# Kernel optimization log

Measured on AMD Instinct MI355X. Metric: run time of the kernel, lower is better.

Reference implementation:

```python
import jax, jax.numpy as jnp
import numpy as np

H = 1024        # bridge_hidden_dim
NH = 16         # num_attention_heads
HD = H // NH    # head_dim = 64
B, S = 4, 1024
PHYS_W = 0.2
CONS_W = 0.15


def setup_inputs() -> dict:
    key = jax.random.key(0)
    ks = jax.random.split(key, 16)
    sc = 0.02
    return {
        "cnn_features": jax.random.normal(ks[0], (B, S, H), jnp.float32),
        "llm_features": jax.random.normal(ks[1], (B, S, H), jnp.float32),
        "Wq": jax.random.normal(ks[2], (H, H), jnp.float32) * sc,
        "bq": jnp.zeros((H,), jnp.float32),
        "Wk": jax.random.normal(ks[3], (H, H), jnp.float32) * sc,
        "bk": jnp.zeros((H,), jnp.float32),
        "Wv": jax.random.normal(ks[4], (H, H), jnp.float32) * sc,
        "bv": jnp.zeros((H,), jnp.float32),
        "Wo": jax.random.normal(ks[5], (H, H), jnp.float32) * sc,
        "bo": jnp.zeros((H,), jnp.float32),
        "ln_g": jnp.ones((H,), jnp.float32),
        "ln_b": jnp.zeros((H,), jnp.float32),
        "e_energy": jax.random.normal(ks[6], (H,), jnp.float32),
        "e_mass": jax.random.normal(ks[7], (H,), jnp.float32),
        "e_momentum": jax.random.normal(ks[8], (H,), jnp.float32),
    }


def _layernorm(x, g, b, eps=1e-5):
    mu = jnp.mean(x, axis=-1, keepdims=True)
    var = jnp.var(x, axis=-1, keepdims=True)
    return (x - mu) * jax.lax.rsqrt(var + eps) * g + b


def _split_heads(x):
    b, s, _ = x.shape
    return x.reshape(b, s, NH, HD).transpose(0, 2, 1, 3)  # [b, h, s, d]


def _physics_attention(q_in, k_in, v_in, Wq, bq, Wk, bk, Wv, bv, Wo, bo, ln_g, ln_b):
    # q_in: [b, sq, H]; k_in == v_in: [b, sk, H] with sq == sk (required by bias math)
    Q = _split_heads(q_in @ Wq.T + bq)  # [b,h,s,d]
    K = _split_heads(k_in @ Wk.T + bk)
    V = _split_heads(v_in @ Wv.T + bv)
    scores = jnp.einsum('bhqd,bhkd->bhqk', Q, K) / jnp.sqrt(jnp.float32(HD))
    # physics constraints (broadcast [b,h,s,1] over key axis)
    energy_bias = jnp.sum(Q * K, axis=-1, keepdims=True) * PHYS_W
    mass_bias = jnp.mean(Q + K, axis=-1, keepdims=True) * CONS_W
    scores = scores + energy_bias + mass_bias
    attn = jax.nn.softmax(scores, axis=-1)  # dropout is identity in eval
    att = jnp.einsum('bhqk,bhkd->bhqd', attn, V)
    b, h, s, d = att.shape
    att = att.transpose(0, 2, 1, 3).reshape(b, s, h * d)
    out = att @ Wo.T + bo
    return _layernorm(q_in + out, ln_g, ln_b)


def reference(cnn_features, llm_features, Wq, bq, Wk, bk, Wv, bv, Wo, bo,
              ln_g, ln_b, e_energy, e_mass, e_momentum):
    b = cnn_features.shape[0]
    phys = jnp.stack([e_energy, e_mass, e_momentum], axis=0)  # [3, H]
    phys = jnp.broadcast_to(phys[None], (b, 3, H))
    aug_cnn = jnp.concatenate([cnn_features, phys], axis=1)  # [b, S+3, H]
    aug_llm = jnp.concatenate([llm_features, phys], axis=1)
    cnn_att = _physics_attention(aug_cnn, aug_llm, aug_llm,
                                 Wq, bq, Wk, bk, Wv, bv, Wo, bo, ln_g, ln_b)
    llm_att = _physics_attention(aug_llm, aug_cnn, aug_cnn,
                                 Wq, bq, Wk, bk, Wv, bv, Wo, bo, ln_g, ln_b)
    cnn_out = cnn_att[:, :cnn_features.shape[1], :]
    llm_out = llm_att[:, :llm_features.shape[1], :]
    return (cnn_out, llm_out)
```

## Files before the change

### kernel.cpp

```cpp
#include <hip/hip_runtime.h>
#include <stdint.h>

#define SA 1027
#define SPAD 1088

typedef __attribute__((ext_vector_type(8))) short short8;
typedef __attribute__((ext_vector_type(4))) float f32x4;
typedef __attribute__((ext_vector_type(2))) unsigned int u32x2;

typedef const __attribute__((address_space(1))) uint8_t* gas1;
typedef __attribute__((address_space(3))) uint8_t* las3;

__device__ __forceinline__ void gload16(const void* g, void* l){
  __builtin_amdgcn_global_load_lds((gas1)g, (las3)l, 16, 0, 0);
}

__device__ __forceinline__ uint16_t f2bf(float f){
  uint32_t x = __builtin_bit_cast(uint32_t, f);
  x = (x + 0x7fffu + ((x >> 16) & 1u)) >> 16;
  return (uint16_t)x;
}
__device__ __forceinline__ float bf2f(uint16_t u){
  uint32_t x = ((uint32_t)u) << 16;
  return __builtin_bit_cast(float, x);
}

__device__ __forceinline__ f32x4 mfma16(short8 a, short8 b, f32x4 c){
  return __builtin_amdgcn_mfma_f32_16x16x32_bf16(a, b, c, 0, 0, 0);
}

#define QSCALE 0.18033688011112042f

__global__ __launch_bounds__(256) void prep_wb(
    const float* __restrict__ Wq, const float* __restrict__ Wk,
    const float* __restrict__ Wv, const float* __restrict__ Wo,
    const float* __restrict__ bq, const float* __restrict__ bk,
    const float* __restrict__ bv, const float* __restrict__ bo,
    uint16_t* __restrict__ W, float* __restrict__ bias){
  const int gid = blockIdx.x*256 + threadIdx.x;
  if (gid < 1048576){
    const int w = gid >> 18;
    const int off = (gid & 262143) << 2;
    const float* src = (w==0) ? Wq : (w==1) ? Wk : (w==2) ? Wv : Wo;
    const float4 v = *(const float4*)(src + off);
    ushort4 u;
    u.x = f2bf(v.x); u.y = f2bf(v.y); u.z = f2bf(v.z); u.w = f2bf(v.w);
    *(ushort4*)(W + ((size_t)w << 20) + off) = u;
  } else if (gid < 1048576 + 1024){
    const int i = (gid - 1048576) << 2;
    const int w = i >> 10;
    const int off = i & 1023;
    const float* src = (w==0) ? bq : (w==1) ? bk : (w==2) ? bv : bo;
    *(float4*)(bias + i) = *(const float4*)(src + off);
  }
}

__global__ __launch_bounds__(256) void prep_X(
    const float* __restrict__ cnn, const float* __restrict__ llm,
    uint16_t* __restrict__ X){
  const int row = blockIdx.x*2 + (threadIdx.x >> 7);
  const int c8 = (threadIdx.x & 127) << 3;
  const int cb = row >> 10, s = row & 1023;
  const int c = cb >> 2, b = cb & 3;
  const float* src = (c ? llm : cnn) + ((size_t)(b*1024 + s))*1024 + c8;
  const float4 v0 = *(const float4*)src;
  const float4 v1 = *(const float4*)(src + 4);
  short8 u;
  u[0]=(short)f2bf(v0.x); u[1]=(short)f2bf(v0.y); u[2]=(short)f2bf(v0.z); u[3]=(short)f2bf(v0.w);
  u[4]=(short)f2bf(v1.x); u[5]=(short)f2bf(v1.y); u[6]=(short)f2bf(v1.z); u[7]=(short)f2bf(v1.w);
  *(short8*)(X + (size_t)row*1024 + c8) = u;
}

__global__ __launch_bounds__(256) void phys_qkv(
    const float* __restrict__ ee, const float* __restrict__ em,
    const float* __restrict__ ep, const uint16_t* __restrict__ W,
    const float* __restrict__ bias, uint16_t* __restrict__ Yqk,
    uint16_t* __restrict__ Vt){
  __shared__ float xs[1024];
  const int t = blockIdx.x >> 3;
  const int col = 1024 + (blockIdx.x & 7)*256 + threadIdx.x;
  const float* e = (t==0) ? ee : (t==1) ? em : ep;
  for (int k = threadIdx.x; k < 1024; k += 256) xs[k] = bf2f(f2bf(e[k]));
  __syncthreads();
  const uint16_t* wr = W + (size_t)col*1024;
  float acc = 0.f;
  for (int k = 0; k < 1024; k += 8){
    const short8 w8 = *(const short8*)(wr + k);
    #pragma unroll
    for (int u = 0; u < 8; ++u) acc += bf2f((uint16_t)w8[u]) * xs[k+u];
  }
  const uint16_t o = f2bf(acc + bias[col]);
  if (col < 2048){
    #pragma unroll
    for (int cb = 0; cb < 8; ++cb)
      Yqk[((size_t)cb*SA + 1024 + t)*2048 + col] = o;
  } else {
    const int hd = col - 2048;
    #pragma unroll
    for (int cb = 0; cb < 8; ++cb)
      Vt[((size_t)(cb*1024 + hd))*SPAD + 1024 + t] = o;
  }
}

__global__ __launch_bounds__(512) void qkv256(
    const uint16_t* __restrict__ A, const uint16_t* __restrict__ B,
    const float* __restrict__ bias, uint16_t* __restrict__ Yqk,
    uint16_t* __restrict__ Vt){
  extern __shared__ uint8_t lds[];
  const int tid = threadIdx.x;
  const int lane = tid & 63, wid = tid >> 6;
  const int l15 = lane & 15, l4 = lane >> 4;
  const int wm = wid >> 2, wn = wid & 3;
  const int wg = (blockIdx.x & 7)*48 + (blockIdx.x >> 3);
  const int bm = wg / 12, bn = wg % 12;

  const uint16_t* Ag = A + (size_t)bm*256*1024;
  const uint16_t* Bg = B + (size_t)bn*256*1024;

  const int srow8 = lane >> 3;
  const int gch = (lane & 7) ^ srow8;
  const int c0 = wid*2, c1 = c0 + 1;
  const size_t ga0 = (size_t)(c0*8 + srow8)*1024 + gch*8;
  const size_t ga1 = (size_t)(c1*8 + srow8)*1024 + gch*8;

#define STG_A(buf, H, kt) do { \
    gload16(Ag + (size_t)(H)*131072 + (size_t)(kt)*64 + ga0, lds + (buf)*65536 + (H)*16384 + c0*1024); \
    gload16(Ag + (size_t)(H)*131072 + (size_t)(kt)*64 + ga1, lds + (buf)*65536 + (H)*16384 + c1*1024); \
  } while(0)
#define STG_B(buf, H, kt) do { \
    gload16(Bg + (size_t)(H)*131072 + (size_t)(kt)*64 + ga0, lds + (buf)*65536 + 32768 + (H)*16384 + c0*1024); \
    gload16(Bg + (size_t)(H)*131072 + (size_t)(kt)*64 + ga1, lds + (buf)*65536 + 32768 + (H)*16384 + c1*1024); \
  } while(0)

  int koff[2];
  koff[0] = (l4*16) ^ ((l15 & 7) << 4);
  koff[1] = (64 + l4*16) ^ ((l15 & 7) << 4);
  const int arow = (wm*128 + l15) * 128;
  const int brow = (wn*64 + l15) * 128;

  f32x4 acc[8][4];
  #pragma unroll
  for (int i = 0; i < 8; ++i)
    #pragma unroll
    for (int j = 0; j < 4; ++j) acc[i][j] = (f32x4){0.f,0.f,0.f,0.f};

  const int NT = 16;
  STG_A(0,0,0); STG_A(0,1,0); STG_B(0,0,0); STG_B(0,1,0);
  STG_A(1,0,1); STG_A(1,1,1); STG_B(1,0,1); STG_B(1,1,1);
  asm volatile("s_waitcnt vmcnt(8)" ::: "memory");
  __builtin_amdgcn_s_barrier();

  for (int s = 0; s < NT; ++s){
    const int b = s & 1;
    const uint8_t* La = lds + b*65536;
    const uint8_t* Lb = La + 32768;
    short8 af[4][2], bf0[2][2], bf1[2][2];

    #pragma unroll
    for (int i = 0; i < 4; ++i){
      af[i][0] = *(const short8*)(La + arow + i*2048 + koff[0]);
      af[i][1] = *(const short8*)(La + arow + i*2048 + koff[1]);
    }
    #pragma unroll
    for (int j = 0; j < 2; ++j){
      bf0[j][0] = *(const short8*)(Lb + brow + j*2048 + koff[0]);
      bf0[j][1] = *(const short8*)(Lb + brow + j*2048 + koff[1]);
    }
    __builtin_amdgcn_s_barrier();
    asm volatile("s_waitcnt lgkmcnt(0)" ::: "memory");
    __builtin_amdgcn_s_setprio(1);
    #pragma unroll
    for (int i = 0; i < 4; ++i)
      #pragma unroll
      for (int j = 0; j < 2; ++j)
        acc[i][j] = mfma16(af[i][1], bf0[j][1], mfma16(af[i][0], bf0[j][0], acc[i][j]));
    __builtin_amdgcn_s_setprio(0);
    __builtin_amdgcn_s_barrier();

    #pragma unroll
    for (int j = 0; j < 2; ++j){
      bf1[j][0] = *(const short8*)(Lb + brow + (j+2)*2048 + koff[0]);
      bf1[j][1] = *(const short8*)(Lb + brow + (j+2)*2048 + koff[1]);
    }
    __builtin_amdgcn_s_barrier();
    asm volatile("s_waitcnt lgkmcnt(0)" ::: "memory");
    __builtin_amdgcn_s_setprio(1);
    #pragma unroll
    for (int i = 0; i < 4; ++i)
      #pragma unroll
      for (int j = 0; j < 2; ++j)
        acc[i][j+2] = mfma16(af[i][1], bf1[j][1], mfma16(af[i][0], bf1[j][0], acc[i][j+2]));
    __builtin_amdgcn_s_setprio(0);
    __builtin_amdgcn_s_barrier();

    #pragma unroll
    for (int i = 0; i < 4; ++i){
      af[i][0] = *(const short8*)(La + 8192 + arow + i*2048 + koff[0]);
      af[i][1] = *(const short8*)(La + 8192 + arow + i*2048 + koff[1]);
    }
    if (s <= NT-3){ STG_B(b, 0, s+2); STG_B(b, 1, s+2); }
    __builtin_amdgcn_s_barrier();
    asm volatile("s_waitcnt lgkmcnt(0)" ::: "memory");
    __builtin_amdgcn_s_setprio(1);
    #pragma unroll
    for (int i = 0; i < 4; ++i)
      #pragma unroll
      for (int j = 0; j < 2; ++j)
        acc[i+4][j+2] = mfma16(af[i][1], bf1[j][1], mfma16(af[i][0], bf1[j][0], acc[i+4][j+2]));
    __builtin_amdgcn_s_setprio(0);
    __builtin_amdgcn_s_barrier();

    if (s <= NT-3){ STG_A(b, 0, s+2); STG_A(b, 1, s+2); }
    __builtin_amdgcn_s_barrier();
    __builtin_amdgcn_s_setprio(1);
    #pragma unroll
    for (int i = 0; i < 4; ++i)
      #pragma unroll
      for (int j = 0; j < 2; ++j)
        acc[i+4][j] = mfma16(af[i][1], bf0[j][1], mfma16(af[i][0], bf0[j][0], acc[i+4][j]));
    __builtin_amdgcn_s_setprio(0);
    if (s <= NT-3)      asm volatile("s_waitcnt vmcnt(8)" ::: "memory");
    else if (s == NT-2) asm volatile("s_waitcnt vmcnt(0)" ::: "memory");
    __builtin_amdgcn_s_barrier();
  }

  #pragma unroll
  for (int j = 0; j < 4; ++j){
    const int n = bn*256 + wn*64 + j*16 + l15;
    const float bb = bias[n];
    if (n < 2048){
      const float sc = (n < 1024) ? QSCALE : 1.0f;
      #pragma unroll
      for (int i = 0; i < 8; ++i){
        const int m0 = bm*256 + wm*128 + i*16 + l4*4;
        #pragma unroll
        for (int r = 0; r < 4; ++r){
          const int m = m0 + r;
          Yqk[((size_t)(m >> 10)*SA + (m & 1023))*2048 + n] = f2bf((acc[i][j][r] + bb) * sc);
        }
      }
    } else {
      const int hd = n - 2048;
      #pragma unroll
      for (int i = 0; i < 8; ++i){
        const int m0 = bm*256 + wm*128 + i*16 + l4*4;
        const size_t vrow = (size_t)(m0 >> 10)*1024 + hd;
        const uint32_t w0 = (uint32_t)f2bf(acc[i][j][0] + bb) | ((uint32_t)f2bf(acc[i][j][1] + bb) << 16);
        const uint32_t w1 = (uint32_t)f2bf(acc[i][j][2] + bb) | ((uint32_t)f2bf(acc[i][j][3] + bb) << 16);
        *(u32x2*)(Vt + vrow*SPAD + (m0 & 1023)) = (u32x2){w0, w1};
      }
    }
  }
#undef STG_A
#undef STG_B
}

__global__ __launch_bounds__(512) void oproj256(
    const uint16_t* __restrict__ A, const uint16_t* __restrict__ B,
    const float* __restrict__ bias, uint16_t* __restrict__ C){
  extern __shared__ uint8_t lds[];
  const int tid = threadIdx.x;
  const int lane = tid & 63, wid = tid >> 6;
  const int l15 = lane & 15, l4 = lane >> 4;
  const int wm = wid >> 2, wn = wid & 3;
  const int wg = (blockIdx.x & 7)*32 + (blockIdx.x >> 3);
  const int bm = wg >> 3, bn = wg & 7;

  const uint16_t* Ag = A + (size_t)bm*256*1024;
  const uint16_t* Bg = B + (size_t)bn*128*1024;

  const int srow8 = lane >> 3;
  const int gch = (lane & 7) ^ srow8;
  const int c0 = wid*2, c1 = c0 + 1;
  const size_t ga0 = (size_t)(c0*8 + srow8)*1024 + gch*8;
  const size_t ga1 = (size_t)(c1*8 + srow8)*1024 + gch*8;

#define STG_A(buf, H, kt) do { \
    gload16(Ag + (size_t)(H)*131072 + (size_t)(kt)*64 + ga0, lds + (buf)*49152 + (H)*16384 + c0*1024); \
    gload16(Ag + (size_t)(H)*131072 + (size_t)(kt)*64 + ga1, lds + (buf)*49152 + (H)*16384 + c1*1024); \
  } while(0)
#define STG_B(buf, kt) do { \
    gload16(Bg + (size_t)(kt)*64 + ga0, lds + (buf)*49152 + 32768 + c0*1024); \
    gload16(Bg + (size_t)(kt)*64 + ga1, lds + (buf)*49152 + 32768 + c1*1024); \
  } while(0)

  int koff[2];
  koff[0] = (l4*16) ^ ((l15 & 7) << 4);
  koff[1] = (64 + l4*16) ^ ((l15 & 7) << 4);
  const int abase = wm*16384 + l15*128;
  const int bbase = 32768 + (wn*32 + l15)*128;

  f32x4 acc[8][2];
  #pragma unroll
  for (int i = 0; i < 8; ++i){ acc[i][0] = (f32x4){0,0,0,0}; acc[i][1] = (f32x4){0,0,0,0}; }

  const int NT = 16;
  STG_A(0,0,0); STG_A(0,1,0); STG_B(0,0);
  STG_A(1,0,1); STG_A(1,1,1); STG_B(1,1);
  asm volatile("s_waitcnt vmcnt(6)" ::: "memory");
  __builtin_amdgcn_s_barrier();

  for (int s = 0; s < NT; ++s){
    const int b = s & 1;
    const uint8_t* L = lds + b*49152;
    short8 af[4][2], af2[4][2], bfr[2][2];

    #pragma unroll
    for (int i = 0; i < 4; ++i){
      af[i][0] = *(const short8*)(L + abase + i*2048 + koff[0]);
      af[i][1] = *(const short8*)(L + abase + i*2048 + koff[1]);
    }
    bfr[0][0] = *(const short8*)(L + bbase + koff[0]);
    bfr[0][1] = *(const short8*)(L + bbase + koff[1]);
    __builtin_amdgcn_s_barrier();
    asm volatile("s_waitcnt lgkmcnt(0)" ::: "memory");
    __builtin_amdgcn_s_setprio(1);
    #pragma unroll
    for (int i = 0; i < 4; ++i)
      acc[i][0] = mfma16(af[i][1], bfr[0][1], mfma16(af[i][0], bfr[0][0], acc[i][0]));
    __builtin_amdgcn_s_setprio(0);
    __builtin_amdgcn_s_barrier();

    bfr[1][0] = *(const short8*)(L + bbase + 2048 + koff[0]);
    bfr[1][1] = *(const short8*)(L + bbase + 2048 + koff[1]);
    __builtin_amdgcn_s_barrier();
    asm volatile("s_waitcnt lgkmcnt(0)" ::: "memory");
    __builtin_amdgcn_s_setprio(1);
    #pragma unroll
    for (int i = 0; i < 4; ++i)
      acc[i][1] = mfma16(af[i][1], bfr[1][1], mfma16(af[i][0], bfr[1][0], acc[i][1]));
    __builtin_amdgcn_s_setprio(0);
    __builtin_amdgcn_s_barrier();

    #pragma unroll
    for (int i = 0; i < 4; ++i){
      af2[i][0] = *(const short8*)(L + abase + 8192 + i*2048 + koff[0]);
      af2[i][1] = *(const short8*)(L + abase + 8192 + i*2048 + koff[1]);
    }
    if (s <= NT-3){ STG_B(b, s+2); }
    __builtin_amdgcn_s_barrier();
    asm volatile("s_waitcnt lgkmcnt(0)" ::: "memory");
    __builtin_amdgcn_s_setprio(1);
    #pragma unroll
    for (int i = 0; i < 4; ++i)
      acc[i+4][1] = mfma16(af2[i][1], bfr[1][1], mfma16(af2[i][0], bfr[1][0], acc[i+4][1]));
    __builtin_amdgcn_s_setprio(0);
    __builtin_amdgcn_s_barrier();

    if (s <= NT-3){ STG_A(b, 0, s+2); STG_A(b, 1, s+2); }
    __builtin_amdgcn_s_barrier();
    __builtin_amdgcn_s_setprio(1);
    #pragma unroll
    for (int i = 0; i < 4; ++i)
      acc[i+4][0] = mfma16(af2[i][1], bfr[0][1], mfma16(af2[i][0], bfr[0][0], acc[i+4][0]));
    __builtin_amdgcn_s_setprio(0);
    if (s <= NT-3)      asm volatile("s_waitcnt vmcnt(6)" ::: "memory");
    else if (s == NT-2) asm volatile("s_waitcnt vmcnt(0)" ::: "memory");
    __builtin_amdgcn_s_barrier();
  }

  #pragma unroll
  for (int j = 0; j < 2; ++j){
    const int n = bn*128 + wn*32 + j*16 + l15;
    const float bb = bias[n];
    #pragma unroll
    for (int i = 0; i < 8; ++i){
      const size_t m0 = (size_t)bm*256 + wm*128 + i*16 + l4*4;
      #pragma unroll
      for (int r = 0; r < 4; ++r)
        C[(m0 + r)*1024 + n] = f2bf(acc[i][j][r] + bb);
    }
  }
#undef STG_A
#undef STG_B
}

__global__ __launch_bounds__(512, 4) void attn_k(
    const uint16_t* __restrict__ Yqk, const uint16_t* __restrict__ Vt,
    uint16_t* __restrict__ att){
  extern __shared__ uint8_t lds[];
  const int tid = threadIdx.x;
  const int lane = tid & 63, wid = tid >> 6;
  const int l15 = lane & 15, l4 = lane >> 4;
  const int i = blockIdx.x;
  const int inst = (i & 7)*16 + ((i >> 3) & 15);
  const int qb = i >> 7;
  const int h = inst & 15, cb = inst >> 4;
  const size_t yrow0 = (size_t)cb * SA;
  const int q0 = qb*256 + wid*32;
  const size_t vbase = (size_t)inst * 64 * SPAD;
  const uint16_t* Yk = Yqk + yrow0*2048 + 1024 + h*64;

  short8 qf[2][2];
  #pragma unroll
  for (int u = 0; u < 2; ++u){
    const uint16_t* p = Yqk + (yrow0 + q0 + u*16 + l15)*2048 + h*64 + l4*8;
    qf[u][0] = *(const short8*)p;
    qf[u][1] = *(const short8*)(p + 32);
  }

  f32x4 o0[4], o1[4];
  float psum0 = 0.f, psum1 = 0.f;
  #pragma unroll
  for (int d = 0; d < 4; ++d){ o0[d] = (f32x4){0,0,0,0}; o1[d] = (f32x4){0,0,0,0}; }

  int koff[2], koffp[2], pwo[4];
  #pragma unroll
  for (int kk = 0; kk < 2; ++kk){
    koff[kk]  = (l15*128 + kk*64 + l4*16) ^ ((l15 & 7) << 4);
    koffp[kk] = l15*144 + kk*64 + l4*16;
  }
  #pragma unroll
  for (int nt = 0; nt < 4; ++nt)
    pwo[nt] = l15*144 + nt*32 + l4*8;
  uint8_t* const pb = lds + 49152 + wid*2304;

  const int srow = lane >> 3, schunk = lane & 7;
  const int strow = wid*8 + srow;
  const int sgch = schunk ^ srow;

#define ASTAGE(t3, kt) do { \
    gload16(Yk + (size_t)((kt)*64 + strow)*2048 + sgch*8, lds + (t3)*8192 + wid*1024); \
    gload16(Vt + vbase + (size_t)strow*SPAD + (kt)*64 + sgch*8, lds + 24576 + (t3)*8192 + wid*1024); \
  } while(0)

  ASTAGE(0, 0);
  ASTAGE(1, 1);
  asm volatile("s_waitcnt vmcnt(2)" ::: "memory");
  __builtin_amdgcn_s_barrier();

  for (int kt = 0; kt < 17; ++kt){
    const int c3 = kt % 3;
    if (kt <= 14){ const int t3 = (kt + 2) % 3; ASTAGE(t3, kt + 2); }
    const uint8_t* bK = lds + c3*8192;
    const uint8_t* bV = lds + 24576 + c3*8192;

    f32x4 sa[4], sb[4];
    #pragma unroll
    for (int nt = 0; nt < 4; ++nt){
      const short8 k0 = *(const short8*)(bK + nt*2048 + koff[0]);
      const short8 k1 = *(const short8*)(bK + nt*2048 + koff[1]);
      sa[nt] = mfma16(k1, qf[0][1], mfma16(k0, qf[0][0], (f32x4){0,0,0,0}));
      sb[nt] = mfma16(k1, qf[1][1], mfma16(k0, qf[1][0], (f32x4){0,0,0,0}));
    }
    if (kt == 16){
      #pragma unroll
      for (int nt = 0; nt < 4; ++nt)
        #pragma unroll
        for (int r = 0; r < 4; ++r){
          if (nt*16 + l4*4 + r >= 3){ sa[nt][r] = -3e38f; sb[nt][r] = -3e38f; }
        }
    }
    #pragma unroll
    for (int nt = 0; nt < 4; ++nt){
      const float p0 = __builtin_amdgcn_exp2f(sa[nt][0]);
      const float p1 = __builtin_amdgcn_exp2f(sa[nt][1]);
      const float p2 = __builtin_amdgcn_exp2f(sa[nt][2]);
      const float p3 = __builtin_amdgcn_exp2f(sa[nt][3]);
      psum0 += (p0 + p1) + (p2 + p3);
      uint32_t w0, w1;
      asm("v_cvt_pk_bf16_f32 %0, %1, %2" : "=v"(w0) : "v"(p0), "v"(p1));
      asm("v_cvt_pk_bf16_f32 %0, %1, %2" : "=v"(w1) : "v"(p2), "v"(p3));
      *(u32x2*)(pb + pwo[nt]) = (u32x2){w0, w1};
    }
    short8 vf[4][2];
    #pragma unroll
    for (int dt = 0; dt < 4; ++dt){
      vf[dt][0] = *(const short8*)(bV + dt*2048 + koff[0]);
      vf[dt][1] = *(const short8*)(bV + dt*2048 + koff[1]);
    }
    #pragma unroll
    for (int kk = 0; kk < 2; ++kk){
      const short8 pf = *(const short8*)(pb + koffp[kk]);
      #pragma unroll
      for (int dt = 0; dt < 4; ++dt)
        o0[dt] = mfma16(pf, vf[dt][kk], o0[dt]);
    }
    #pragma unroll
    for (int nt = 0; nt < 4; ++nt){
      const float p0 = __builtin_amdgcn_exp2f(sb[nt][0]);
      const float p1 = __builtin_amdgcn_exp2f(sb[nt][1]);
      const float p2 = __builtin_amdgcn_exp2f(sb[nt][2]);
      const float p3 = __builtin_amdgcn_exp2f(sb[nt][3]);
      psum1 += (p0 + p1) + (p2 + p3);
      uint32_t w0, w1;
      asm("v_cvt_pk_bf16_f32 %0, %1, %2" : "=v"(w0) : "v"(p0), "v"(p1));
      asm("v_cvt_pk_bf16_f32 %0, %1, %2" : "=v"(w1) : "v"(p2), "v"(p3));
      *(u32x2*)(pb + pwo[nt]) = (u32x2){w0, w1};
    }
    #pragma unroll
    for (int kk = 0; kk < 2; ++kk){
      const short8 pf = *(const short8*)(pb + koffp[kk]);
      #pragma unroll
      for (int dt = 0; dt < 4; ++dt)
        o1[dt] = mfma16(pf, vf[dt][kk], o1[dt]);
    }
    if (kt <= 14)      asm volatile("s_waitcnt vmcnt(2)" ::: "memory");
    else if (kt == 15) asm volatile("s_waitcnt vmcnt(0)" ::: "memory");
    if (kt <= 15) __builtin_amdgcn_s_barrier();
  }
#undef ASTAGE

  psum0 += __shfl_xor(psum0, 16); psum0 += __shfl_xor(psum0, 32);
  psum1 += __shfl_xor(psum1, 16); psum1 += __shfl_xor(psum1, 32);
  const size_t arow0 = (size_t)cb*1024 + q0;
  #pragma unroll
  for (int r = 0; r < 4; ++r){
    const float inv0 = 1.f / __shfl(psum0, l4*4 + r);
    const float inv1 = 1.f / __shfl(psum1, l4*4 + r);
    #pragma unroll
    for (int dt = 0; dt < 4; ++dt){
      att[(arow0 + l4*4 + r)*1024 + h*64 + dt*16 + l15] = f2bf(o0[dt][r] * inv0);
      att[(arow0 + 16 + l4*4 + r)*1024 + h*64 + dt*16 + l15] = f2bf(o1[dt][r] * inv1);
    }
  }
}

__global__ __launch_bounds__(256) void ln_out(
    const uint16_t* __restrict__ Op, const float* __restrict__ cnn,
    const float* __restrict__ llm, const float* __restrict__ g,
    const float* __restrict__ b, float* __restrict__ out){
  const int row = blockIdx.x;
  const int c = row >> 12, bq = row & 4095;
  const int tid = threadIdx.x;
  const ushort4 u = *(const ushort4*)(Op + (size_t)row*1024 + (tid<<2));
  const float4 rv = *(const float4*)((c ? llm : cnn) + (size_t)bq*1024 + (tid<<2));
  const float x0 = bf2f(u.x) + rv.x;
  const float x1 = bf2f(u.y) + rv.y;
  const float x2 = bf2f(u.z) + rv.z;
  const float x3 = bf2f(u.w) + rv.w;
  float s1 = x0+x1+x2+x3;
  float s2 = x0*x0+x1*x1+x2*x2+x3*x3;
  #pragma unroll
  for (int m=1;m<64;m<<=1){ s1 += __shfl_xor(s1,m); s2 += __shfl_xor(s2,m); }
  __shared__ float r1[4], r2[4];
  const int wid = tid >> 6, lane = tid & 63;
  if (lane == 0){ r1[wid] = s1; r2[wid] = s2; }
  __syncthreads();
  s1 = r1[0]+r1[1]+r1[2]+r1[3];
  s2 = r2[0]+r2[1]+r2[2]+r2[3];
  const float mu = s1 * 0.0009765625f;
  const float var = s2 * 0.0009765625f - mu*mu;
  const float rs = rsqrtf(var + 1e-5f);
  const float4 gv = *(const float4*)(g + (tid<<2));
  const float4 bv = *(const float4*)(b + (tid<<2));
  float4 ov;
  ov.x = (x0 - mu)*rs*gv.x + bv.x;
  ov.y = (x1 - mu)*rs*gv.y + bv.y;
  ov.z = (x2 - mu)*rs*gv.z + bv.z;
  ov.w = (x3 - mu)*rs*gv.w + bv.w;
  *(float4*)(out + ((size_t)c << 22) + (size_t)bq*1024 + (tid<<2)) = ov;
}

extern "C" void kernel_launch(void* const* d_in, const int* in_sizes, int n_in,
                              void* d_out, int out_size, void* d_ws, size_t ws_size,
                              hipStream_t stream){
  const float* cnn = (const float*)d_in[0];
  const float* llm = (const float*)d_in[1];
  const float* Wq  = (const float*)d_in[2];
  const float* bq  = (const float*)d_in[3];
  const float* Wk  = (const float*)d_in[4];
  const float* bk  = (const float*)d_in[5];
  const float* Wv  = (const float*)d_in[6];
  const float* bv  = (const float*)d_in[7];
  const float* Wo  = (const float*)d_in[8];
  const float* bo  = (const float*)d_in[9];
  const float* lng = (const float*)d_in[10];
  const float* lnb = (const float*)d_in[11];
  const float* ee  = (const float*)d_in[12];
  const float* em  = (const float*)d_in[13];
  const float* ep  = (const float*)d_in[14];

  uint8_t* ws = (uint8_t*)d_ws;
  uint16_t* X    = (uint16_t*)(ws + 0);
  uint16_t* W    = (uint16_t*)(ws + 16777216);
  float*    bias = (float*)   (ws + 25165824);
  uint16_t* Yqk  = (uint16_t*)(ws + 25182208);
  uint16_t* Vt   = (uint16_t*)(ws + 59785216);
  uint16_t* att  = X;
  uint16_t* Op   = Yqk;
  float* out = (float*)d_out;

  hipFuncSetAttribute((const void*)qkv256,
                      hipFuncAttributeMaxDynamicSharedMemorySize, 131072);
  hipFuncSetAttribute((const void*)oproj256,
                      hipFuncAttributeMaxDynamicSharedMemorySize, 98304);
  hipFuncSetAttribute((const void*)attn_k,
                      hipFuncAttributeMaxDynamicSharedMemorySize, 67584);

  prep_wb<<<4100, 256, 0, stream>>>(Wq, Wk, Wv, Wo, bq, bk, bv, bo, W, bias);
  prep_X<<<4096, 256, 0, stream>>>(cnn, llm, X);
  phys_qkv<<<24, 256, 0, stream>>>(ee, em, ep, W, bias, Yqk, Vt);
  qkv256<<<384, 512, 131072, stream>>>(X, W, bias, Yqk, Vt);
  attn_k<<<512, 512, 67584, stream>>>(Yqk, Vt, att);
  oproj256<<<256, 512, 98304, stream>>>(att, W + 3145728, bias + 3072, Op);
  ln_out<<<8192, 256, 0, stream>>>(Op, cnn, llm, lng, lnb, out);
}
```

Measured before the change: 189.8 us.

## Restructure GEMM prefetch schedule: stage A one tile ahead, B two ahead, occupancy hint

Changes the global-to-LDS prefetch schedule in the QKV and output-projection GEMMs. A tiles are now loaded one k-step ahead into the other buffer and B tiles two steps ahead, spread across the phases of each iteration. Tail iterations issue redundant reloads of the current step instead of being guarded by branches. The output-projection loop is cut from four MFMA phases to two, which removes barriers. Both kernels get launch_bounds(512,2) to ask for two workgroups per CU, at the cost of register pressure and possible write-after-read hazards on the reused LDS buffers.

```diff
diff --git a/kernel.cpp b/kernel.cpp
--- a/kernel.cpp
+++ b/kernel.cpp
@@ -102,7 +102,7 @@
   }
 }
 
-__global__ __launch_bounds__(512) void qkv256(
+__global__ __launch_bounds__(512, 2) void qkv256(
     const uint16_t* __restrict__ A, const uint16_t* __restrict__ B,
     const float* __restrict__ bias, uint16_t* __restrict__ Yqk,
     uint16_t* __restrict__ Vt){
@@ -146,16 +146,20 @@
 
   const int NT = 16;
   STG_A(0,0,0); STG_A(0,1,0); STG_B(0,0,0); STG_B(0,1,0);
-  STG_A(1,0,1); STG_A(1,1,1); STG_B(1,0,1); STG_B(1,1,1);
-  asm volatile("s_waitcnt vmcnt(8)" ::: "memory");
+  STG_B(1,0,1); STG_B(1,1,1);
+  asm volatile("s_waitcnt vmcnt(4)" ::: "memory");
   __builtin_amdgcn_s_barrier();
 
   for (int s = 0; s < NT; ++s){
     const int b = s & 1;
     const uint8_t* La = lds + b*65536;
     const uint8_t* Lb = La + 32768;
+    const int sn1 = (s+1 < NT) ? s+1 : s;
+    const int sn2 = (s+2 < NT) ? s+2 : s;
+    const int nb = b ^ 1;
     short8 af[4][2], bf0[2][2], bf1[2][2];
 
+    STG_A(nb, 0, sn1);
     #pragma unroll
     for (int i = 0; i < 4; ++i){
       af[i][0] = *(const short8*)(La + arow + i*2048 + koff[0]);
@@ -177,6 +181,7 @@
     __builtin_amdgcn_s_setprio(0);
     __builtin_amdgcn_s_barrier();
 
+    STG_A(nb, 1, sn1);
     #pragma unroll
     for (int j = 0; j < 2; ++j){
       bf1[j][0] = *(const short8*)(Lb + brow + (j+2)*2048 + koff[0]);
@@ -193,12 +198,12 @@
     __builtin_amdgcn_s_setprio(0);
     __builtin_amdgcn_s_barrier();
 
+    STG_B(b, 0, sn2);
     #pragma unroll
     for (int i = 0; i < 4; ++i){
       af[i][0] = *(const short8*)(La + 8192 + arow + i*2048 + koff[0]);
       af[i][1] = *(const short8*)(La + 8192 + arow + i*2048 + koff[1]);
     }
-    if (s <= NT-3){ STG_B(b, 0, s+2); STG_B(b, 1, s+2); }
     __builtin_amdgcn_s_barrier();
     asm volatile("s_waitcnt lgkmcnt(0)" ::: "memory");
     __builtin_amdgcn_s_setprio(1);
@@ -210,7 +215,7 @@
     __builtin_amdgcn_s_setprio(0);
     __builtin_amdgcn_s_barrier();
 
-    if (s <= NT-3){ STG_A(b, 0, s+2); STG_A(b, 1, s+2); }
+    STG_B(b, 1, sn2);
     __builtin_amdgcn_s_barrier();
     __builtin_amdgcn_s_setprio(1);
     #pragma unroll
@@ -219,8 +224,7 @@
       for (int j = 0; j < 2; ++j)
         acc[i+4][j] = mfma16(af[i][1], bf0[j][1], mfma16(af[i][0], bf0[j][0], acc[i+4][j]));
     __builtin_amdgcn_s_setprio(0);
-    if (s <= NT-3)      asm volatile("s_waitcnt vmcnt(8)" ::: "memory");
-    else if (s == NT-2) asm volatile("s_waitcnt vmcnt(0)" ::: "memory");
+    asm volatile("s_waitcnt vmcnt(4)" ::: "memory");
     __builtin_amdgcn_s_barrier();
   }
 
@@ -255,7 +259,7 @@
 #undef STG_B
 }
 
-__global__ __launch_bounds__(512) void oproj256(
+__global__ __launch_bounds__(512, 2) void oproj256(
     const uint16_t* __restrict__ A, const uint16_t* __restrict__ B,
     const float* __restrict__ bias, uint16_t* __restrict__ C){
   extern __shared__ uint8_t lds[];
@@ -295,67 +299,56 @@
   for (int i = 0; i < 8; ++i){ acc[i][0] = (f32x4){0,0,0,0}; acc[i][1] = (f32x4){0,0,0,0}; }
 
   const int NT = 16;
-  STG_A(0,0,0); STG_A(0,1,0); STG_B(0,0);
-  STG_A(1,0,1); STG_A(1,1,1); STG_B(1,1);
-  asm volatile("s_waitcnt vmcnt(6)" ::: "memory");
+  STG_A(0,0,0); STG_A(0,1,0); STG_B(0,0); STG_B(1,1);
+  asm volatile("s_waitcnt vmcnt(2)" ::: "memory");
   __builtin_amdgcn_s_barrier();
 
   for (int s = 0; s < NT; ++s){
-    const int b = s & 1;
+    const int b = s & 1, nb = b ^ 1;
     const uint8_t* L = lds + b*49152;
-    short8 af[4][2], af2[4][2], bfr[2][2];
-
+    const int sn1 = (s+1 < NT) ? s+1 : s;
+    const int sn2 = (s+2 < NT) ? s+2 : s;
+    short8 af[4][2], bfr[2][2];
+
+    STG_A(nb, 0, sn1);
     #pragma unroll
     for (int i = 0; i < 4; ++i){
       af[i][0] = *(const short8*)(L + abase + i*2048 + koff[0]);
       af[i][1] = *(const short8*)(L + abase + i*2048 + koff[1]);
     }
-    bfr[0][0] = *(const short8*)(L + bbase + koff[0]);
-    bfr[0][1] = *(const short8*)(L + bbase + koff[1]);
+    #pragma unroll
+    for (int j = 0; j < 2; ++j){
+      bfr[j][0] = *(const short8*)(L + bbase + j*2048 + koff[0]);
+      bfr[j][1] = *(const short8*)(L + bbase + j*2048 + koff[1]);
+    }
     __builtin_amdgcn_s_barrier();
     asm volatile("s_waitcnt lgkmcnt(0)" ::: "memory");
     __builtin_amdgcn_s_setprio(1);
     #pragma unroll
     for (int i = 0; i < 4; ++i)
-      acc[i][0] = mfma16(af[i][1], bfr[0][1], mfma16(af[i][0], bfr[0][0], acc[i][0]));
+      #pragma unroll
+      for (int j = 0; j < 2; ++j)
+        acc[i][j] = mfma16(af[i][1], bfr[j][1], mfma16(af[i][0], bfr[j][0], acc[i][j]));
     __builtin_amdgcn_s_setprio(0);
     __builtin_amdgcn_s_barrier();
 
-    bfr[1][0] = *(const short8*)(L + bbase + 2048 + koff[0]);
-    bfr[1][1] = *(const short8*)(L + bbase + 2048 + koff[1]);
+    STG_A(nb, 1, sn1);
+    STG_B(b, sn2);
+    #pragma unroll
+    for (int i = 0; i < 4; ++i){
+      af[i][0] = *(const short8*)(L + abase + 8192 + i*2048 + koff[0]);
+      af[i][1] = *(const short8*)(L + abase + 8192 + i*2048 + koff[1]);
+    }
     __builtin_amdgcn_s_barrier();
     asm volatile("s_waitcnt lgkmcnt(0)" ::: "memory");
     __builtin_amdgcn_s_setprio(1);
     #pragma unroll
     for (int i = 0; i < 4; ++i)
-      acc[i][1] = mfma16(af[i][1], bfr[1][1], mfma16(af[i][0], bfr[1][0], acc[i][1]));
+      #pragma unroll
+      for (int j = 0; j < 2; ++j)
+        acc[i+4][j] = mfma16(af[i][1], bfr[j][1], mfma16(af[i][0], bfr[j][0], acc[i+4][j]));
     __builtin_amdgcn_s_setprio(0);
-    __builtin_amdgcn_s_barrier();
-
-    #pragma unroll
-    for (int i = 0; i < 4; ++i){
-      af2[i][0] = *(const short8*)(L + abase + 8192 + i*2048 + koff[0]);
-      af2[i][1] = *(const short8*)(L + abase + 8192 + i*2048 + koff[1]);
-    }
-    if (s <= NT-3){ STG_B(b, s+2); }
-    __builtin_amdgcn_s_barrier();
-    asm volatile("s_waitcnt lgkmcnt(0)" ::: "memory");
-    __builtin_amdgcn_s_setprio(1);
-    #pragma unroll
-    for (int i = 0; i < 4; ++i)
-      acc[i+4][1] = mfma16(af2[i][1], bfr[1][1], mfma16(af2[i][0], bfr[1][0], acc[i+4][1]));
-    __builtin_amdgcn_s_setprio(0);
-    __builtin_amdgcn_s_barrier();
-
-    if (s <= NT-3){ STG_A(b, 0, s+2); STG_A(b, 1, s+2); }
-    __builtin_amdgcn_s_barrier();
-    __builtin_amdgcn_s_setprio(1);
-    #pragma unroll
-    for (int i = 0; i < 4; ++i)
-      acc[i+4][0] = mfma16(af2[i][1], bfr[0][1], mfma16(af2[i][0], bfr[0][0], acc[i+4][0]));
-    __builtin_amdgcn_s_setprio(0);
-    if (s <= NT-3)      asm volatile("s_waitcnt vmcnt(6)" ::: "memory");
-    else if (s == NT-2) asm volatile("s_waitcnt vmcnt(0)" ::: "memory");
+    asm volatile("s_waitcnt vmcnt(2)" ::: "memory");
     __builtin_amdgcn_s_barrier();
   }
 
```

After: 186.6 us. Within noise of the previous version (-1.7%).
